# Optimization experiments

Measured on AMD Instinct MI355X. Metric: run time of the kernel, lower is better.

## Reference

```python
import jax, jax.numpy as jnp
import numpy as np

VOCAB, EMBED, HIDDEN = 50000, 256, 512
B, SEQ = 64, 200


def setup_inputs() -> dict:
    key = jax.random.key(0)
    ks = jax.random.split(key, 16)
    h2 = 2 * HIDDEN
    inp = {
        "input_idx": jax.random.randint(ks[0], (B,), 0, VOCAB),
        "encoded": jax.random.normal(ks[1], (B, SEQ, h2), jnp.float32),
        "encoded_idx": jax.random.randint(ks[2], (B, SEQ), 0, VOCAB),
        "prev_state": jax.random.normal(ks[3], (B, HIDDEN), jnp.float32),
        "weighted": jax.random.normal(ks[4], (B, 1, h2), jnp.float32),
        "order": 1,
        # learned parameters
        "embed_table": jax.random.normal(ks[5], (VOCAB, EMBED), jnp.float32) * 0.02,
        "w_ih": jax.random.normal(ks[6], (3 * HIDDEN, EMBED + h2), jnp.float32) * 0.02,
        "w_hh": jax.random.normal(ks[7], (3 * HIDDEN, HIDDEN), jnp.float32) * 0.02,
        "b_ih": jax.random.normal(ks[8], (3 * HIDDEN,), jnp.float32) * 0.02,
        "b_hh": jax.random.normal(ks[9], (3 * HIDDEN,), jnp.float32) * 0.02,
        "wo_w": jax.random.normal(ks[10], (VOCAB, HIDDEN), jnp.float32) * 0.02,
        "wo_b": jax.random.normal(ks[11], (VOCAB,), jnp.float32) * 0.02,
        "wc_w": jax.random.normal(ks[12], (HIDDEN, h2), jnp.float32) * 0.02,
        "wc_b": jax.random.normal(ks[13], (HIDDEN,), jnp.float32) * 0.02,
    }
    return inp


def _gru_step(x, h, w_ih, w_hh, b_ih, b_hh):
    # torch GRU gate ordering: reset, update, new
    gx = x @ w_ih.T + b_ih            # [b, 3h]
    gh = h @ w_hh.T + b_hh            # [b, 3h]
    xr, xz, xn = jnp.split(gx, 3, axis=-1)
    hr, hz, hn = jnp.split(gh, 3, axis=-1)
    r = jax.nn.sigmoid(xr + hr)
    z = jax.nn.sigmoid(xz + hz)
    n = jnp.tanh(xn + r * hn)
    return (1.0 - z) * n + z * h


def reference(input_idx, encoded, encoded_idx, prev_state, weighted, order,
              embed_table, w_ih, w_hh, b_ih, b_hh, wo_w, wo_b, wc_w, wc_b):
    b, seq, _ = encoded.shape
    vocab = wo_w.shape[0]

    # GRU single step on [embed(input); weighted]
    x = jnp.concatenate([embed_table[input_idx], weighted[:, 0, :]], axis=-1)
    state = _gru_step(x, prev_state, w_ih, w_hh, b_ih, b_hh)  # [b, h]

    # generate score over vocab
    score_g = state @ wo_w.T + wo_b                           # [b, vocab]

    # copy score over source positions
    score_c = jnp.tanh(jnp.einsum('bsk,hk->bsh', encoded, wc_w) + wc_b)
    score_c = jnp.einsum('bsh,bh->bs', score_c, state)        # [b, seq]

    encoded_mask = (encoded_idx != 0).astype(score_c.dtype)
    idx_from_input = (encoded_idx == input_idx[:, None]).astype(score_c.dtype)
    score_c = score_c * encoded_mask * idx_from_input

    # joint softmax over [vocab + seq]
    probs = jax.nn.softmax(jnp.concatenate([score_g, score_c], axis=1), axis=1)
    prob_g = probs[:, :vocab]
    prob_c = probs[:, vocab:]                                 # [b, seq]

    # scatter copy probs into vocab space (equivalent to one-hot bmm)
    flat_idx = (jnp.arange(b)[:, None] * vocab + encoded_idx).reshape(-1)
    prob_c_to_g = jnp.zeros((b * vocab,), probs.dtype).at[flat_idx].add(
        prob_c.reshape(-1)).reshape(b, vocab)

    out = (prob_g + prob_c_to_g)[:, None, :]                  # [b, 1, vocab]

    # selective-read attention, renormalized where sum > 0 (detached divisor)
    attn = prob_c * idx_from_input
    s = jax.lax.stop_gradient(jnp.sum(attn, axis=1, keepdims=True))
    attn = jnp.where(s > 0.0, attn / jnp.where(s > 0.0, s, 1.0), attn)
    weighted_new = jnp.einsum('bs,bsk->bk', attn, encoded)[:, None, :]  # [b,1,2h]

    return out, state, weighted_new
```

## Files before the change

### kernel.cpp

```cpp
#include <hip/hip_runtime.h>
#include <hip/hip_bf16.h>
#include <cstdint>
#include <cstddef>

#define VOCAB  50000
#define EMBED  256
#define HIDDEN 512
#define BATCH  64
#define SEQ    200
#define H2     1024
#define XDIM   1280
#define G3     1536
#define NPART  8
#define V4     (VOCAB/4)
#define CHUNK4 1563

typedef __attribute__((ext_vector_type(8))) short short8;
typedef __attribute__((ext_vector_type(4))) float f32x4;

__device__ __forceinline__ short f2bf(float f) {
  uint32_t u = __builtin_bit_cast(uint32_t, f);
  uint32_t r = (u + 0x7fffu + ((u >> 16) & 1u)) >> 16;
  return (short)(r & 0xffffu);
}

__device__ __forceinline__ void omerge(float& m, float& s, float m2, float s2) {
  if (m2 > m) { s = s * __expf(m - m2) + s2; m = m2; }
  else if (m2 != -INFINITY) { s += s2 * __expf(m2 - m); }
}

__launch_bounds__(256)
__global__ void gru_gemm(const int* __restrict__ idx, const float* __restrict__ embed,
                         const float* __restrict__ weighted, const float* __restrict__ h0,
                         const float* __restrict__ w_ih, const float* __restrict__ w_hh,
                         float* __restrict__ gxp, float* __restrict__ ghp) {
  __shared__ __align__(16) short As[4 * 64 * 8];
  const int tid  = threadIdx.x;
  const int wave = tid >> 6, lane = tid & 63;
  const int l15  = lane & 15, lk = lane >> 4;
  const int slice = blockIdx.y;
  const bool isX  = slice < 8;
  const float* B  = isX ? w_ih : w_hh;
  const int ldb   = isX ? XDIM : HIDDEN;
  const int kbeg  = isX ? slice * 160 : (slice - 8) * 128;
  const int kend  = kbeg + (isX ? 160 : 128);
  float* C = isX ? (gxp + (size_t)slice * BATCH * G3)
                 : (ghp + (size_t)(slice - 8) * BATCH * G3);
  const int ncol = blockIdx.x * 64 + wave * 16;

  f32x4 acc0 = {0,0,0,0}, acc1 = {0,0,0,0}, acc2 = {0,0,0,0}, acc3 = {0,0,0,0};

  const int sl  = tid & 63;
  const int sm  = (tid >> 6) * 16 + (sl & 15);
  const int skb = (sl >> 4) * 8;

  const int nrow = ncol + l15;
  const float* Bbase = B + (size_t)nrow * ldb + lk * 8;

  for (int kc = kbeg; kc < kend; kc += 32) {
    {
      const float4* ap;
      if (isX) {
        int col = kc + skb;
        if (col < EMBED) ap = reinterpret_cast<const float4*>(embed + (size_t)idx[sm] * EMBED + col);
        else             ap = reinterpret_cast<const float4*>(weighted + (size_t)sm * H2 + (col - EMBED));
      } else {
        ap = reinterpret_cast<const float4*>(h0 + (size_t)sm * HIDDEN + kc + skb);
      }
      float4 v0 = ap[0], v1 = ap[1];
      short8 fr;
      fr[0]=f2bf(v0.x); fr[1]=f2bf(v0.y); fr[2]=f2bf(v0.z); fr[3]=f2bf(v0.w);
      fr[4]=f2bf(v1.x); fr[5]=f2bf(v1.y); fr[6]=f2bf(v1.z); fr[7]=f2bf(v1.w);
      *reinterpret_cast<short8*>(&As[tid * 8]) = fr;
    }
    __syncthreads();
    short8 bf;
    {
      const float4* bp = reinterpret_cast<const float4*>(Bbase + kc);
      float4 v0 = bp[0], v1 = bp[1];
      bf[0]=f2bf(v0.x); bf[1]=f2bf(v0.y); bf[2]=f2bf(v0.z); bf[3]=f2bf(v0.w);
      bf[4]=f2bf(v1.x); bf[5]=f2bf(v1.y); bf[6]=f2bf(v1.z); bf[7]=f2bf(v1.w);
    }
    short8 a0 = *reinterpret_cast<const short8*>(&As[(0*64 + lane)*8]);
    short8 a1 = *reinterpret_cast<const short8*>(&As[(1*64 + lane)*8]);
    short8 a2 = *reinterpret_cast<const short8*>(&As[(2*64 + lane)*8]);
    short8 a3 = *reinterpret_cast<const short8*>(&As[(3*64 + lane)*8]);
    acc0 = __builtin_amdgcn_mfma_f32_16x16x32_bf16(a0, bf, acc0, 0, 0, 0);
    acc1 = __builtin_amdgcn_mfma_f32_16x16x32_bf16(a1, bf, acc1, 0, 0, 0);
    acc2 = __builtin_amdgcn_mfma_f32_16x16x32_bf16(a2, bf, acc2, 0, 0, 0);
    acc3 = __builtin_amdgcn_mfma_f32_16x16x32_bf16(a3, bf, acc3, 0, 0, 0);
    __syncthreads();
  }

  const int n = ncol + l15;
  #pragma unroll
  for (int r = 0; r < 4; ++r) {
    C[(size_t)(0*16 + lk*4 + r) * G3 + n] = acc0[r];
    C[(size_t)(1*16 + lk*4 + r) * G3 + n] = acc1[r];
    C[(size_t)(2*16 + lk*4 + r) * G3 + n] = acc2[r];
    C[(size_t)(3*16 + lk*4 + r) * G3 + n] = acc3[r];
  }
}

__launch_bounds__(256)
__global__ void gemm_vocab(const float* __restrict__ A,
                           const float* __restrict__ B,
                           const float* __restrict__ bias,
                           float* __restrict__ C) {
  __shared__ __align__(16) short As[4 * 64 * 8];
  const int tid  = threadIdx.x;
  const int wave = tid >> 6, lane = tid & 63;
  const int l15  = lane & 15, lk = lane >> 4;
  const int ncol = blockIdx.x * 64 + wave * 16;

  f32x4 acc0 = {0,0,0,0}, acc1 = {0,0,0,0}, acc2 = {0,0,0,0}, acc3 = {0,0,0,0};

  const int sl  = tid & 63;
  const int sm  = (tid >> 6) * 16 + (sl & 15);
  const int skb = (sl >> 4) * 8;

  int nrow = ncol + l15; if (nrow > VOCAB - 1) nrow = VOCAB - 1;
  const float* Bbase = B + (size_t)nrow * HIDDEN + lk * 8;

  for (int kc = 0; kc < HIDDEN; kc += 32) {
    {
      const float4* ap = reinterpret_cast<const float4*>(A + (size_t)sm * HIDDEN + kc + skb);
      float4 v0 = ap[0], v1 = ap[1];
      short8 fr;
      fr[0]=f2bf(v0.x); fr[1]=f2bf(v0.y); fr[2]=f2bf(v0.z); fr[3]=f2bf(v0.w);
      fr[4]=f2bf(v1.x); fr[5]=f2bf(v1.y); fr[6]=f2bf(v1.z); fr[7]=f2bf(v1.w);
      *reinterpret_cast<short8*>(&As[tid * 8]) = fr;
    }
    __syncthreads();
    short8 bf;
    {
      const float4* bp = reinterpret_cast<const float4*>(Bbase + kc);
      float4 v0 = bp[0], v1 = bp[1];
      bf[0]=f2bf(v0.x); bf[1]=f2bf(v0.y); bf[2]=f2bf(v0.z); bf[3]=f2bf(v0.w);
      bf[4]=f2bf(v1.x); bf[5]=f2bf(v1.y); bf[6]=f2bf(v1.z); bf[7]=f2bf(v1.w);
    }
    short8 a0 = *reinterpret_cast<const short8*>(&As[(0*64 + lane)*8]);
    short8 a1 = *reinterpret_cast<const short8*>(&As[(1*64 + lane)*8]);
    short8 a2 = *reinterpret_cast<const short8*>(&As[(2*64 + lane)*8]);
    short8 a3 = *reinterpret_cast<const short8*>(&As[(3*64 + lane)*8]);
    acc0 = __builtin_amdgcn_mfma_f32_16x16x32_bf16(a0, bf, acc0, 0, 0, 0);
    acc1 = __builtin_amdgcn_mfma_f32_16x16x32_bf16(a1, bf, acc1, 0, 0, 0);
    acc2 = __builtin_amdgcn_mfma_f32_16x16x32_bf16(a2, bf, acc2, 0, 0, 0);
    acc3 = __builtin_amdgcn_mfma_f32_16x16x32_bf16(a3, bf, acc3, 0, 0, 0);
    __syncthreads();
  }

  const int n = ncol + l15;
  if (n < VOCAB) {
    float bv = bias[n];
    #pragma unroll
    for (int r = 0; r < 4; ++r) {
      C[(size_t)(0*16 + lk*4 + r) * VOCAB + n] = acc0[r] + bv;
      C[(size_t)(1*16 + lk*4 + r) * VOCAB + n] = acc1[r] + bv;
      C[(size_t)(2*16 + lk*4 + r) * VOCAB + n] = acc2[r] + bv;
      C[(size_t)(3*16 + lk*4 + r) * VOCAB + n] = acc3[r] + bv;
    }
  }
}

__launch_bounds__(256)
__global__ void gru_gates(const float* __restrict__ gxp, const float* __restrict__ ghp,
                          const float* __restrict__ b_ih, const float* __restrict__ b_hh,
                          const float* __restrict__ h0, float* __restrict__ out_state) {
  int i = blockIdx.x * 256 + threadIdx.x;
  int b = i >> 9, h = i & 511;
  float xr = b_ih[h], xz = b_ih[HIDDEN + h], xn = b_ih[2*HIDDEN + h];
  #pragma unroll
  for (int s = 0; s < 8; ++s) {
    const float* g = gxp + (size_t)s * BATCH * G3 + (size_t)b * G3;
    xr += g[h]; xz += g[HIDDEN + h]; xn += g[2*HIDDEN + h];
  }
  float hr = b_hh[h], hz = b_hh[HIDDEN + h], hn = b_hh[2*HIDDEN + h];
  #pragma unroll
  for (int s = 0; s < 4; ++s) {
    const float* g = ghp + (size_t)s * BATCH * G3 + (size_t)b * G3;
    hr += g[h]; hz += g[HIDDEN + h]; hn += g[2*HIDDEN + h];
  }
  float r = 1.f / (1.f + __expf(-(xr + hr)));
  float z = 1.f / (1.f + __expf(-(xz + hz)));
  float n = tanhf(xn + r * hn);
  out_state[(size_t)b*HIDDEN + h] = (1.f - z) * n + z * h0[(size_t)b*HIDDEN + h];
}

__launch_bounds__(256)
__global__ void stats_scc(const float* __restrict__ Sg, const int* __restrict__ eidx,
                          const int* __restrict__ iidx, const float* __restrict__ enc,
                          const float* __restrict__ wc_w, const float* __restrict__ wc_b,
                          const float* __restrict__ state,
                          float* __restrict__ scc, float* __restrict__ pstats) {
  __shared__ int   act[SEQ];
  __shared__ float red[256];
  __shared__ float ms[4], ss[4];
  const int b = blockIdx.x >> 3, part = blockIdx.x & 7;
  const int tid = threadIdx.x;

  if (part == 0) {
    int in0 = iidx[b];
    if (tid < SEQ) {
      int e = eidx[b*SEQ + tid];
      act[tid] = (e != 0 && e == in0);
      scc[b*SEQ + tid] = 0.f;
    }
    __syncthreads();
    for (int sq = 0; sq < SEQ; ++sq) {
      if (act[sq]) {
        const float4* er = reinterpret_cast<const float4*>(enc + (size_t)b*SEQ*H2 + (size_t)sq*H2);
        float part_sum = 0.f;
        for (int h = tid; h < HIDDEN; h += 256) {
          const float4* wr = reinterpret_cast<const float4*>(wc_w + (size_t)h*H2);
          float d = wc_b[h];
          for (int k = 0; k < H2/4; ++k) {
            float4 a = er[k], w = wr[k];
            d += a.x*w.x + a.y*w.y + a.z*w.z + a.w*w.w;
          }
          part_sum += tanhf(d) * state[(size_t)b*HIDDEN + h];
        }
        red[tid] = part_sum;
        __syncthreads();
        for (int off = 128; off > 0; off >>= 1) {
          if (tid < off) red[tid] += red[tid + off];
          __syncthreads();
        }
        if (tid == 0) scc[b*SEQ + sq] = red[0];
        __syncthreads();
      }
    }
    __syncthreads();
  }

  float m = -INFINITY, s = 0.f;
  const float4* p = reinterpret_cast<const float4*>(Sg + (size_t)b*VOCAB);
  const int i0 = part * CHUNK4;
  const int i1 = (i0 + CHUNK4 < V4) ? i0 + CHUNK4 : V4;
  for (int i = i0 + tid; i < i1; i += 256) {
    float4 v = p[i];
    omerge(m, s, v.x, 1.f); omerge(m, s, v.y, 1.f);
    omerge(m, s, v.z, 1.f); omerge(m, s, v.w, 1.f);
  }
  if (part == 0) {
    for (int i = tid; i < SEQ; i += 256) omerge(m, s, scc[b*SEQ + i], 1.f);
  }
  for (int off = 1; off < 64; off <<= 1) {
    float m2 = __shfl_xor(m, off), s2 = __shfl_xor(s, off);
    omerge(m, s, m2, s2);
  }
  int wave = tid >> 6, lane = tid & 63;
  if (lane == 0) { ms[wave] = m; ss[wave] = s; }
  __syncthreads();
  if (tid == 0) {
    float M = ms[0], S = ss[0];
    for (int w = 1; w < 4; ++w) omerge(M, S, ms[w], ss[w]);
    pstats[b*2*NPART + part*2]     = M;
    pstats[b*2*NPART + part*2 + 1] = S;
  }
}

__device__ __forceinline__ void merge_stats(const float* __restrict__ pstats, int b,
                                            float& M, float& S) {
  M = -INFINITY; S = 0.f;
  #pragma unroll
  for (int p = 0; p < NPART; ++p)
    omerge(M, S, pstats[b*2*NPART + 2*p], pstats[b*2*NPART + 2*p + 1]);
}

__launch_bounds__(256)
__global__ void finalize_out(const float* __restrict__ Sg, const float* __restrict__ pstats,
                             float* __restrict__ out0) {
  int g = blockIdx.x * 256 + threadIdx.x;
  int b = g / V4, i = g - b * V4;
  float M, S; merge_stats(pstats, b, M, S);
  float inv = 1.f / S;
  float4 v = reinterpret_cast<const float4*>(Sg + (size_t)b*VOCAB)[i];
  float4 o;
  o.x = __expf(v.x - M) * inv; o.y = __expf(v.y - M) * inv;
  o.z = __expf(v.z - M) * inv; o.w = __expf(v.w - M) * inv;
  reinterpret_cast<float4*>(out0 + (size_t)b*VOCAB)[i] = o;
}

__launch_bounds__(256)
__global__ void epilogue(const int* __restrict__ eidx, const int* __restrict__ iidx,
                         const float* __restrict__ scc, const float* __restrict__ pstats,
                         const float* __restrict__ enc, float* __restrict__ out0,
                         float* __restrict__ wnew) {
  int b = blockIdx.x, tid = threadIdx.x;
  __shared__ float attn_sh[SEQ];
  __shared__ float fnorm_sh;
  float M, S; merge_stats(pstats, b, M, S);
  float inv = 1.f / S;
  int in0 = iidx[b];
  if (tid < SEQ) {
    int e = eidx[b*SEQ + tid];
    float p = __expf(scc[b*SEQ + tid] - M) * inv;
    atomicAdd(&out0[(size_t)b*VOCAB + e], p);
    attn_sh[tid] = (e == in0) ? p : 0.f;
  }
  __syncthreads();
  if (tid == 0) {
    float s = 0.f;
    for (int i = 0; i < SEQ; ++i) s += attn_sh[i];
    fnorm_sh = (s > 0.f) ? 1.f / s : 1.f;
  }
  __syncthreads();
  float f = fnorm_sh;
  float a0 = 0, a1 = 0, a2 = 0, a3 = 0;
  const float4* ep = reinterpret_cast<const float4*>(enc + (size_t)b*SEQ*H2);
  for (int s = 0; s < SEQ; ++s) {
    float a = attn_sh[s];
    if (a != 0.f) {
      a *= f;
      float4 v = ep[(size_t)s*(H2/4) + tid];
      a0 += a*v.x; a1 += a*v.y; a2 += a*v.z; a3 += a*v.w;
    }
  }
  float4 o = {a0, a1, a2, a3};
  reinterpret_cast<float4*>(wnew + (size_t)b*H2)[tid] = o;
}

extern "C" void kernel_launch(void* const* d_in, const int* in_sizes, int n_in,
                              void* d_out, int out_size, void* d_ws, size_t ws_size,
                              hipStream_t stream) {
  (void)in_sizes; (void)n_in; (void)out_size; (void)ws_size;
  const int*   input_idx  = (const int*)d_in[0];
  const float* encoded    = (const float*)d_in[1];
  const int*   enc_idx    = (const int*)d_in[2];
  const float* prev_state = (const float*)d_in[3];
  const float* weighted   = (const float*)d_in[4];
  const float* embed      = (const float*)d_in[6];
  const float* w_ih       = (const float*)d_in[7];
  const float* w_hh       = (const float*)d_in[8];
  const float* b_ih       = (const float*)d_in[9];
  const float* b_hh       = (const float*)d_in[10];
  const float* wo_w       = (const float*)d_in[11];
  const float* wo_b       = (const float*)d_in[12];
  const float* wc_w       = (const float*)d_in[13];
  const float* wc_b       = (const float*)d_in[14];

  float* out0      = (float*)d_out;
  float* out_state = out0 + (size_t)BATCH * VOCAB;
  float* out_wnew  = out_state + BATCH * HIDDEN;

  float* ws    = (float*)d_ws;
  float* gxp   = ws;
  float* ghp   = ws + (size_t)8 * BATCH * G3;
  float* Sg    = ws;
  float* scc   = ws + (size_t)BATCH * VOCAB;
  float* pstats= scc + BATCH * SEQ;

  gru_gemm<<<dim3(G3/64, 12), 256, 0, stream>>>(input_idx, embed, weighted, prev_state,
                                                w_ih, w_hh, gxp, ghp);
  gru_gates<<<(BATCH*HIDDEN)/256, 256, 0, stream>>>(gxp, ghp, b_ih, b_hh, prev_state, out_state);
  gemm_vocab<<<(VOCAB + 63)/64, 256, 0, stream>>>(out_state, wo_w, wo_b, Sg);
  stats_scc<<<BATCH * NPART, 256, 0, stream>>>(Sg, enc_idx, input_idx, encoded,
                                               wc_w, wc_b, out_state, scc, pstats);
  finalize_out<<<(BATCH*VOCAB/4)/256, 256, 0, stream>>>(Sg, pstats, out0);
  epilogue<<<BATCH, 256, 0, stream>>>(enc_idx, input_idx, scc, pstats, encoded, out0, out_wnew);
}
```

Baseline: 91.70 us.

## Fuse vocab GEMM with exp and sum, drop max pass, merge scatter into normalize

Measured after the change: 103.1 us. +12.4%, slower.

```diff
diff --git a/kernel.cpp b/kernel.cpp
--- a/kernel.cpp
+++ b/kernel.cpp
@@ -11,9 +11,9 @@
 #define H2     1024
 #define XDIM   1280
 #define G3     1536
-#define NPART  8
 #define V4     (VOCAB/4)
-#define CHUNK4 1563
+#define NVB    782
+#define NFB    49
 
 typedef __attribute__((ext_vector_type(8))) short short8;
 typedef __attribute__((ext_vector_type(4))) float f32x4;
@@ -24,9 +24,11 @@
   return (short)(r & 0xffffu);
 }
 
-__device__ __forceinline__ void omerge(float& m, float& s, float m2, float s2) {
-  if (m2 > m) { s = s * __expf(m - m2) + s2; m = m2; }
-  else if (m2 != -INFINITY) { s += s2 * __expf(m2 - m); }
+__device__ __forceinline__ short8 pack8(float4 v0, float4 v1) {
+  short8 fr;
+  fr[0]=f2bf(v0.x); fr[1]=f2bf(v0.y); fr[2]=f2bf(v0.z); fr[3]=f2bf(v0.w);
+  fr[4]=f2bf(v1.x); fr[5]=f2bf(v1.y); fr[6]=f2bf(v1.z); fr[7]=f2bf(v1.w);
+  return fr;
 }
 
 __launch_bounds__(256)
@@ -67,19 +69,13 @@
       } else {
         ap = reinterpret_cast<const float4*>(h0 + (size_t)sm * HIDDEN + kc + skb);
       }
-      float4 v0 = ap[0], v1 = ap[1];
-      short8 fr;
-      fr[0]=f2bf(v0.x); fr[1]=f2bf(v0.y); fr[2]=f2bf(v0.z); fr[3]=f2bf(v0.w);
-      fr[4]=f2bf(v1.x); fr[5]=f2bf(v1.y); fr[6]=f2bf(v1.z); fr[7]=f2bf(v1.w);
-      *reinterpret_cast<short8*>(&As[tid * 8]) = fr;
+      *reinterpret_cast<short8*>(&As[tid * 8]) = pack8(ap[0], ap[1]);
     }
     __syncthreads();
     short8 bf;
     {
       const float4* bp = reinterpret_cast<const float4*>(Bbase + kc);
-      float4 v0 = bp[0], v1 = bp[1];
-      bf[0]=f2bf(v0.x); bf[1]=f2bf(v0.y); bf[2]=f2bf(v0.z); bf[3]=f2bf(v0.w);
-      bf[4]=f2bf(v1.x); bf[5]=f2bf(v1.y); bf[6]=f2bf(v1.z); bf[7]=f2bf(v1.w);
+      bf = pack8(bp[0], bp[1]);
     }
     short8 a0 = *reinterpret_cast<const short8*>(&As[(0*64 + lane)*8]);
     short8 a1 = *reinterpret_cast<const short8*>(&As[(1*64 + lane)*8]);
@@ -103,71 +99,12 @@
 }
 
 __launch_bounds__(256)
-__global__ void gemm_vocab(const float* __restrict__ A,
-                           const float* __restrict__ B,
-                           const float* __restrict__ bias,
-                           float* __restrict__ C) {
-  __shared__ __align__(16) short As[4 * 64 * 8];
-  const int tid  = threadIdx.x;
-  const int wave = tid >> 6, lane = tid & 63;
-  const int l15  = lane & 15, lk = lane >> 4;
-  const int ncol = blockIdx.x * 64 + wave * 16;
-
-  f32x4 acc0 = {0,0,0,0}, acc1 = {0,0,0,0}, acc2 = {0,0,0,0}, acc3 = {0,0,0,0};
-
-  const int sl  = tid & 63;
-  const int sm  = (tid >> 6) * 16 + (sl & 15);
-  const int skb = (sl >> 4) * 8;
-
-  int nrow = ncol + l15; if (nrow > VOCAB - 1) nrow = VOCAB - 1;
-  const float* Bbase = B + (size_t)nrow * HIDDEN + lk * 8;
-
-  for (int kc = 0; kc < HIDDEN; kc += 32) {
-    {
-      const float4* ap = reinterpret_cast<const float4*>(A + (size_t)sm * HIDDEN + kc + skb);
-      float4 v0 = ap[0], v1 = ap[1];
-      short8 fr;
-      fr[0]=f2bf(v0.x); fr[1]=f2bf(v0.y); fr[2]=f2bf(v0.z); fr[3]=f2bf(v0.w);
-      fr[4]=f2bf(v1.x); fr[5]=f2bf(v1.y); fr[6]=f2bf(v1.z); fr[7]=f2bf(v1.w);
-      *reinterpret_cast<short8*>(&As[tid * 8]) = fr;
-    }
-    __syncthreads();
-    short8 bf;
-    {
-      const float4* bp = reinterpret_cast<const float4*>(Bbase + kc);
-      float4 v0 = bp[0], v1 = bp[1];
-      bf[0]=f2bf(v0.x); bf[1]=f2bf(v0.y); bf[2]=f2bf(v0.z); bf[3]=f2bf(v0.w);
-      bf[4]=f2bf(v1.x); bf[5]=f2bf(v1.y); bf[6]=f2bf(v1.z); bf[7]=f2bf(v1.w);
-    }
-    short8 a0 = *reinterpret_cast<const short8*>(&As[(0*64 + lane)*8]);
-    short8 a1 = *reinterpret_cast<const short8*>(&As[(1*64 + lane)*8]);
-    short8 a2 = *reinterpret_cast<const short8*>(&As[(2*64 + lane)*8]);
-    short8 a3 = *reinterpret_cast<const short8*>(&As[(3*64 + lane)*8]);
-    acc0 = __builtin_amdgcn_mfma_f32_16x16x32_bf16(a0, bf, acc0, 0, 0, 0);
-    acc1 = __builtin_amdgcn_mfma_f32_16x16x32_bf16(a1, bf, acc1, 0, 0, 0);
-    acc2 = __builtin_amdgcn_mfma_f32_16x16x32_bf16(a2, bf, acc2, 0, 0, 0);
-    acc3 = __builtin_amdgcn_mfma_f32_16x16x32_bf16(a3, bf, acc3, 0, 0, 0);
-    __syncthreads();
-  }
-
-  const int n = ncol + l15;
-  if (n < VOCAB) {
-    float bv = bias[n];
-    #pragma unroll
-    for (int r = 0; r < 4; ++r) {
-      C[(size_t)(0*16 + lk*4 + r) * VOCAB + n] = acc0[r] + bv;
-      C[(size_t)(1*16 + lk*4 + r) * VOCAB + n] = acc1[r] + bv;
-      C[(size_t)(2*16 + lk*4 + r) * VOCAB + n] = acc2[r] + bv;
-      C[(size_t)(3*16 + lk*4 + r) * VOCAB + n] = acc3[r] + bv;
-    }
-  }
-}
-
-__launch_bounds__(256)
 __global__ void gru_gates(const float* __restrict__ gxp, const float* __restrict__ ghp,
                           const float* __restrict__ b_ih, const float* __restrict__ b_hh,
-                          const float* __restrict__ h0, float* __restrict__ out_state) {
+                          const float* __restrict__ h0, float* __restrict__ out_state,
+                          float* __restrict__ S) {
   int i = blockIdx.x * 256 + threadIdx.x;
+  if (blockIdx.x == 0 && threadIdx.x < BATCH) S[threadIdx.x] = 0.f;
   int b = i >> 9, h = i & 511;
   float xr = b_ih[h], xz = b_ih[HIDDEN + h], xn = b_ih[2*HIDDEN + h];
   #pragma unroll
@@ -188,23 +125,27 @@
 }
 
 __launch_bounds__(256)
-__global__ void stats_scc(const float* __restrict__ Sg, const int* __restrict__ eidx,
-                          const int* __restrict__ iidx, const float* __restrict__ enc,
-                          const float* __restrict__ wc_w, const float* __restrict__ wc_b,
-                          const float* __restrict__ state,
-                          float* __restrict__ scc, float* __restrict__ pstats) {
+__global__ void vocab_fused(const float* __restrict__ state, const float* __restrict__ wo_w,
+                            const float* __restrict__ wo_b,
+                            const int* __restrict__ eidx, const int* __restrict__ iidx,
+                            const float* __restrict__ enc, const float* __restrict__ wc_w,
+                            const float* __restrict__ wc_b,
+                            float* __restrict__ E, float* __restrict__ escc,
+                            float* __restrict__ S) {
+  __shared__ __align__(16) short As[16 * 4 * 64 * 8];
+  __shared__ float red[256];
+  __shared__ float sval[SEQ];
   __shared__ int   act[SEQ];
-  __shared__ float red[256];
-  __shared__ float ms[4], ss[4];
-  const int b = blockIdx.x >> 3, part = blockIdx.x & 7;
+  const int bid = blockIdx.x;
   const int tid = threadIdx.x;
 
-  if (part == 0) {
-    int in0 = iidx[b];
+  if (bid >= NVB) {
+    const int b = bid - NVB;
+    const int in0 = iidx[b];
     if (tid < SEQ) {
       int e = eidx[b*SEQ + tid];
-      act[tid] = (e != 0 && e == in0);
-      scc[b*SEQ + tid] = 0.f;
+      act[tid]  = (e != 0 && e == in0);
+      sval[tid] = 0.f;
     }
     __syncthreads();
     for (int sq = 0; sq < SEQ; ++sq) {
@@ -226,99 +167,147 @@
           if (tid < off) red[tid] += red[tid + off];
           __syncthreads();
         }
-        if (tid == 0) scc[b*SEQ + sq] = red[0];
+        if (tid == 0) sval[sq] = red[0];
         __syncthreads();
       }
     }
     __syncthreads();
-  }
-
-  float m = -INFINITY, s = 0.f;
-  const float4* p = reinterpret_cast<const float4*>(Sg + (size_t)b*VOCAB);
-  const int i0 = part * CHUNK4;
-  const int i1 = (i0 + CHUNK4 < V4) ? i0 + CHUNK4 : V4;
-  for (int i = i0 + tid; i < i1; i += 256) {
-    float4 v = p[i];
-    omerge(m, s, v.x, 1.f); omerge(m, s, v.y, 1.f);
-    omerge(m, s, v.z, 1.f); omerge(m, s, v.w, 1.f);
-  }
-  if (part == 0) {
-    for (int i = tid; i < SEQ; i += 256) omerge(m, s, scc[b*SEQ + i], 1.f);
-  }
-  for (int off = 1; off < 64; off <<= 1) {
-    float m2 = __shfl_xor(m, off), s2 = __shfl_xor(s, off);
-    omerge(m, s, m2, s2);
-  }
-  int wave = tid >> 6, lane = tid & 63;
-  if (lane == 0) { ms[wave] = m; ss[wave] = s; }
+    float ex = 0.f;
+    if (tid < SEQ) {
+      ex = __expf(sval[tid]);
+      escc[b*SEQ + tid] = ex;
+    }
+    red[tid] = ex;
+    __syncthreads();
+    for (int off = 128; off > 0; off >>= 1) {
+      if (tid < off) red[tid] += red[tid + off];
+      __syncthreads();
+    }
+    if (tid == 0) atomicAdd(&S[b], red[0]);
+    return;
+  }
+
+  #pragma unroll
+  for (int p = 0; p < 16; ++p) {
+    const int f     = p * 256 + tid;
+    const int lanef = f & 63;
+    const int a     = (f >> 6) & 3;
+    const int row   = a*16 + (lanef & 15);
+    const int k     = p*32 + (lanef >> 4) * 8;
+    const float4* ap = reinterpret_cast<const float4*>(state + (size_t)row * HIDDEN + k);
+    *reinterpret_cast<short8*>(&As[f * 8]) = pack8(ap[0], ap[1]);
+  }
   __syncthreads();
-  if (tid == 0) {
-    float M = ms[0], S = ss[0];
-    for (int w = 1; w < 4; ++w) omerge(M, S, ms[w], ss[w]);
-    pstats[b*2*NPART + part*2]     = M;
-    pstats[b*2*NPART + part*2 + 1] = S;
-  }
-}
-
-__device__ __forceinline__ void merge_stats(const float* __restrict__ pstats, int b,
-                                            float& M, float& S) {
-  M = -INFINITY; S = 0.f;
-  #pragma unroll
-  for (int p = 0; p < NPART; ++p)
-    omerge(M, S, pstats[b*2*NPART + 2*p], pstats[b*2*NPART + 2*p + 1]);
+
+  const int wave = tid >> 6, lane = tid & 63;
+  const int l15  = lane & 15, lk = lane >> 4;
+  const int ncol = bid * 64 + wave * 16;
+  int nrow = ncol + l15; if (nrow > VOCAB - 1) nrow = VOCAB - 1;
+  const float* Bb = wo_w + (size_t)nrow * HIDDEN + lk * 8;
+
+  f32x4 acc0 = {0,0,0,0}, acc1 = {0,0,0,0}, acc2 = {0,0,0,0}, acc3 = {0,0,0,0};
+  #pragma unroll 4
+  for (int c = 0; c < 16; ++c) {
+    const float4* bp = reinterpret_cast<const float4*>(Bb + c*32);
+    short8 bf = pack8(bp[0], bp[1]);
+    short8 a0 = *reinterpret_cast<const short8*>(&As[((c*4 + 0)*64 + lane)*8]);
+    short8 a1 = *reinterpret_cast<const short8*>(&As[((c*4 + 1)*64 + lane)*8]);
+    short8 a2 = *reinterpret_cast<const short8*>(&As[((c*4 + 2)*64 + lane)*8]);
+    short8 a3 = *reinterpret_cast<const short8*>(&As[((c*4 + 3)*64 + lane)*8]);
+    acc0 = __builtin_amdgcn_mfma_f32_16x16x32_bf16(a0, bf, acc0, 0, 0, 0);
+    acc1 = __builtin_amdgcn_mfma_f32_16x16x32_bf16(a1, bf, acc1, 0, 0, 0);
+    acc2 = __builtin_amdgcn_mfma_f32_16x16x32_bf16(a2, bf, acc2, 0, 0, 0);
+    acc3 = __builtin_amdgcn_mfma_f32_16x16x32_bf16(a3, bf, acc3, 0, 0, 0);
+  }
+
+  const int n = ncol + l15;
+  const bool valid = n < VOCAB;
+  const float bv = valid ? wo_b[n] : 0.f;
+  f32x4 accs[4] = {acc0, acc1, acc2, acc3};
+  #pragma unroll
+  for (int a = 0; a < 4; ++a) {
+    #pragma unroll
+    for (int r = 0; r < 4; ++r) {
+      float ev = valid ? __expf(accs[a][r] + bv) : 0.f;
+      if (valid) E[(size_t)(a*16 + lk*4 + r) * VOCAB + n] = ev;
+      float v = ev;
+      v += __shfl_xor(v, 1); v += __shfl_xor(v, 2);
+      v += __shfl_xor(v, 4); v += __shfl_xor(v, 8);
+      if (l15 == 0) red[wave*64 + a*16 + lk*4 + r] = v;
+    }
+  }
+  __syncthreads();
+  if (tid < 64)
+    atomicAdd(&S[tid], red[0*64+tid] + red[1*64+tid] + red[2*64+tid] + red[3*64+tid]);
 }
 
 __launch_bounds__(256)
-__global__ void finalize_out(const float* __restrict__ Sg, const float* __restrict__ pstats,
-                             float* __restrict__ out0) {
-  int g = blockIdx.x * 256 + threadIdx.x;
-  int b = g / V4, i = g - b * V4;
-  float M, S; merge_stats(pstats, b, M, S);
-  float inv = 1.f / S;
-  float4 v = reinterpret_cast<const float4*>(Sg + (size_t)b*VOCAB)[i];
-  float4 o;
-  o.x = __expf(v.x - M) * inv; o.y = __expf(v.y - M) * inv;
-  o.z = __expf(v.z - M) * inv; o.w = __expf(v.w - M) * inv;
-  reinterpret_cast<float4*>(out0 + (size_t)b*VOCAB)[i] = o;
-}
-
-__launch_bounds__(256)
-__global__ void epilogue(const int* __restrict__ eidx, const int* __restrict__ iidx,
-                         const float* __restrict__ scc, const float* __restrict__ pstats,
-                         const float* __restrict__ enc, float* __restrict__ out0,
-                         float* __restrict__ wnew) {
-  int b = blockIdx.x, tid = threadIdx.x;
-  __shared__ float attn_sh[SEQ];
-  __shared__ float fnorm_sh;
-  float M, S; merge_stats(pstats, b, M, S);
-  float inv = 1.f / S;
-  int in0 = iidx[b];
-  if (tid < SEQ) {
-    int e = eidx[b*SEQ + tid];
-    float p = __expf(scc[b*SEQ + tid] - M) * inv;
-    atomicAdd(&out0[(size_t)b*VOCAB + e], p);
-    attn_sh[tid] = (e == in0) ? p : 0.f;
-  }
-  __syncthreads();
-  if (tid == 0) {
-    float s = 0.f;
-    for (int i = 0; i < SEQ; ++i) s += attn_sh[i];
-    fnorm_sh = (s > 0.f) ? 1.f / s : 1.f;
-  }
-  __syncthreads();
-  float f = fnorm_sh;
-  float a0 = 0, a1 = 0, a2 = 0, a3 = 0;
-  const float4* ep = reinterpret_cast<const float4*>(enc + (size_t)b*SEQ*H2);
-  for (int s = 0; s < SEQ; ++s) {
-    float a = attn_sh[s];
-    if (a != 0.f) {
-      a *= f;
-      float4 v = ep[(size_t)s*(H2/4) + tid];
-      a0 += a*v.x; a1 += a*v.y; a2 += a*v.z; a3 += a*v.w;
-    }
-  }
-  float4 o = {a0, a1, a2, a3};
-  reinterpret_cast<float4*>(wnew + (size_t)b*H2)[tid] = o;
+__global__ void finalize_fused(const int* __restrict__ eidx, const int* __restrict__ iidx,
+                               const float* __restrict__ escc, const float* __restrict__ S,
+                               const float* __restrict__ enc,
+                               float* __restrict__ out0, float* __restrict__ wnew) {
+  const int bid = blockIdx.x;
+  const int tid = threadIdx.x;
+
+  if (bid < BATCH * NFB) {
+    __shared__ int   me[SEQ];
+    __shared__ float mp[SEQ];
+    __shared__ int   cnt;
+    const int b = bid / NFB, c = bid % NFB;
+    if (tid == 0) cnt = 0;
+    __syncthreads();
+    if (tid < SEQ) {
+      int e = eidx[b*SEQ + tid];
+      if ((e >> 10) == c) {
+        int j = atomicAdd(&cnt, 1);
+        me[j] = e; mp[j] = escc[b*SEQ + tid];
+      }
+    }
+    __syncthreads();
+    const float inv = 1.f / S[b];
+    const int i4 = c * 256 + tid;
+    if (i4 < V4) {
+      float4 v = reinterpret_cast<const float4*>(out0 + (size_t)b*VOCAB)[i4];
+      float4 o;
+      o.x = v.x * inv; o.y = v.y * inv; o.z = v.z * inv; o.w = v.w * inv;
+      const int base = i4 * 4;
+      const int n = cnt;
+      for (int j = 0; j < n; ++j) {
+        unsigned d = (unsigned)(me[j] - base);
+        if (d < 4u) (&o.x)[d] += mp[j] * inv;
+      }
+      reinterpret_cast<float4*>(out0 + (size_t)b*VOCAB)[i4] = o;
+    }
+  } else {
+    __shared__ float attn_sh[SEQ];
+    __shared__ float fnorm_sh;
+    const int b = bid - BATCH * NFB;
+    const int in0 = iidx[b];
+    if (tid < SEQ) {
+      int e = eidx[b*SEQ + tid];
+      attn_sh[tid] = (e == in0) ? escc[b*SEQ + tid] : 0.f;
+    }
+    __syncthreads();
+    if (tid == 0) {
+      float s = 0.f;
+      for (int i = 0; i < SEQ; ++i) s += attn_sh[i];
+      fnorm_sh = (s > 0.f) ? 1.f / s : 1.f;
+    }
+    __syncthreads();
+    const float f = fnorm_sh;
+    float a0 = 0, a1 = 0, a2 = 0, a3 = 0;
+    const float4* ep = reinterpret_cast<const float4*>(enc + (size_t)b*SEQ*H2);
+    for (int s = 0; s < SEQ; ++s) {
+      float a = attn_sh[s];
+      if (a != 0.f) {
+        a *= f;
+        float4 v = ep[(size_t)s*(H2/4) + tid];
+        a0 += a*v.x; a1 += a*v.y; a2 += a*v.z; a3 += a*v.w;
+      }
+    }
+    float4 o = {a0, a1, a2, a3};
+    reinterpret_cast<float4*>(wnew + (size_t)b*H2)[tid] = o;
+  }
 }
 
 extern "C" void kernel_launch(void* const* d_in, const int* in_sizes, int n_in,
@@ -347,16 +336,15 @@
   float* ws    = (float*)d_ws;
   float* gxp   = ws;
   float* ghp   = ws + (size_t)8 * BATCH * G3;
-  float* Sg    = ws;
-  float* scc   = ws + (size_t)BATCH * VOCAB;
-  float* pstats= scc + BATCH * SEQ;
+  float* escc  = ws + (size_t)12 * BATCH * G3;
+  float* S     = escc + BATCH * SEQ;
 
   gru_gemm<<<dim3(G3/64, 12), 256, 0, stream>>>(input_idx, embed, weighted, prev_state,
                                                 w_ih, w_hh, gxp, ghp);
-  gru_gates<<<(BATCH*HIDDEN)/256, 256, 0, stream>>>(gxp, ghp, b_ih, b_hh, prev_state, out_state);
-  gemm_vocab<<<(VOCAB + 63)/64, 256, 0, stream>>>(out_state, wo_w, wo_b, Sg);
-  stats_scc<<<BATCH * NPART, 256, 0, stream>>>(Sg, enc_idx, input_idx, encoded,
-                                               wc_w, wc_b, out_state, scc, pstats);
-  finalize_out<<<(BATCH*VOCAB/4)/256, 256, 0, stream>>>(Sg, pstats, out0);
-  epilogue<<<BATCH, 256, 0, stream>>>(enc_idx, input_idx, scc, pstats, encoded, out0, out_wnew);
-}
+  gru_gates<<<(BATCH*HIDDEN)/256, 256, 0, stream>>>(gxp, ghp, b_ih, b_hh, prev_state,
+                                                    out_state, S);
+  vocab_fused<<<NVB + BATCH, 256, 0, stream>>>(out_state, wo_w, wo_b, enc_idx, input_idx,
+                                               encoded, wc_w, wc_b, out0, escc, S);
+  finalize_fused<<<BATCH*NFB + BATCH, 256, 0, stream>>>(enc_idx, input_idx, escc, S,
+                                                        encoded, out0, out_wnew);
+}
```
